# Optimization experiments

Hardware: AMD Instinct MI355X
Metric: run time of the kernel (lower is better)

## Reference

```python
import jax, jax.numpy as jnp
import numpy as np

DIM = 768
N_HEADS = 12
HEAD_DIM = DIM // N_HEADS
B, S = 2, 4096


def setup_inputs() -> dict:
    key = jax.random.key(0)
    k_x, k_wqkv, k_bqkv, k_wout, k_bout = jax.random.split(key, 5)
    scale_in = 1.0 / np.sqrt(DIM)
    return {
        "x": jax.random.normal(k_x, (B, S, DIM), dtype=jnp.float32),
        "Wqkv": jax.random.normal(k_wqkv, (DIM, 3 * DIM), dtype=jnp.float32) * scale_in,
        "bqkv": jax.random.normal(k_bqkv, (3 * DIM,), dtype=jnp.float32) * 0.02,
        "Wout": jax.random.normal(k_wout, (DIM, DIM), dtype=jnp.float32) * scale_in,
        "bout": jax.random.normal(k_bout, (DIM,), dtype=jnp.float32) * 0.02,
    }


def reference(x, Wqkv, bqkv, Wout, bout):
    b, s, d = x.shape
    qkv = (x @ Wqkv + bqkv).reshape(b, s, 3, N_HEADS, HEAD_DIM)
    qkv = jnp.transpose(qkv, (2, 0, 3, 1, 4))  # [3, B, H, S, hd]
    q, k, v = qkv[0], qkv[1], qkv[2]
    scale = HEAD_DIM ** -0.5
    attn = jnp.einsum('bhqd,bhkd->bhqk', q, k) * scale  # [B, H, S, S]
    causal_mask = jnp.triu(jnp.ones((s, s), dtype=bool), k=1)
    attn = jnp.where(causal_mask[None, None], -jnp.inf, attn)
    attn = jax.nn.softmax(attn, axis=-1)
    out = jnp.einsum('bhqk,bhkd->bhqd', attn, v)  # [B, H, S, hd]
    out = jnp.transpose(out, (0, 2, 1, 3)).reshape(b, s, d)
    return out @ Wout + bout
```

## Files before the change

### kernel.cpp

```cpp
#include <hip/hip_runtime.h>
#include <hip/hip_bf16.h>
#include <math.h>

#define DIM 768
#define NH 12
#define HD 64
#define BATCH 2
#define SEQ 4096
#define MTOT (BATCH * SEQ)

#define QSCALE 0.1803368801111244f

typedef unsigned short u16;
typedef __bf16 bf16x8 __attribute__((ext_vector_type(8)));
typedef float  f32x4  __attribute__((ext_vector_type(4)));
typedef float  f32x16 __attribute__((ext_vector_type(16)));
typedef unsigned short u16x4 __attribute__((ext_vector_type(4)));
typedef unsigned short u16x8 __attribute__((ext_vector_type(8)));
typedef unsigned u32x4 __attribute__((ext_vector_type(4)));

__device__ inline u16 f2bf(float f) {
    unsigned u = __builtin_bit_cast(unsigned, f);
    u += 0x7fffu + ((u >> 16) & 1u);
    return (u16)(u >> 16);
}

#if defined(__has_builtin) && __has_builtin(__builtin_amdgcn_cvt_pk_bf16_f32)
#define HAVE_PK_BF16 1
__device__ inline unsigned pk2bf(float a, float b) {
    auto v = __builtin_amdgcn_cvt_pk_bf16_f32(a, b);
    return __builtin_bit_cast(unsigned, v);
}
#else
#define HAVE_PK_BF16 0
__device__ inline unsigned pk2bf(float a, float b) {
    return (unsigned)f2bf(a) | ((unsigned)f2bf(b) << 16);
}
#endif

__device__ inline f32x4 mfma16(bf16x8 a, bf16x8 b, f32x4 c) {
    return __builtin_amdgcn_mfma_f32_16x16x32_bf16(a, b, c, 0, 0, 0);
}
__device__ inline f32x16 mfma32(bf16x8 a, bf16x8 b, f32x16 c) {
    return __builtin_amdgcn_mfma_f32_32x32x16_bf16(a, b, c, 0, 0, 0);
}

__device__ inline void gl2lds16(const u16* g, u16* l) {
    __builtin_amdgcn_global_load_lds(
        (const __attribute__((address_space(1))) void*)g,
        (__attribute__((address_space(3))) void*)l,
        16, 0, 0);
}

__global__ __launch_bounds__(256)
void cvt_bf16(const float* __restrict__ src, u16* __restrict__ dst, int n8)
{
    int i = blockIdx.x * 256 + threadIdx.x;
    if (i >= n8) return;
    float4 a = ((const float4*)src)[i * 2];
    float4 b = ((const float4*)src)[i * 2 + 1];
    u16x8 o;
    o[0] = f2bf(a.x); o[1] = f2bf(a.y); o[2] = f2bf(a.z); o[3] = f2bf(a.w);
    o[4] = f2bf(b.x); o[5] = f2bf(b.y); o[6] = f2bf(b.z); o[7] = f2bf(b.w);
    ((u16x8*)dst)[i] = o;
}

__global__ __launch_bounds__(256)
void transpose_to_bf16(const float* __restrict__ src, u16* __restrict__ dst,
                       int R, int C)
{
    __shared__ float tile[32][33];
    const int c0 = blockIdx.x * 32, r0 = blockIdx.y * 32;
    const int tx = threadIdx.x & 31, ty = threadIdx.x >> 5;
#pragma unroll
    for (int i = 0; i < 4; ++i) {
        int row = ty * 4 + i;
        tile[row][tx] = src[(size_t)(r0 + row) * C + c0 + tx];
    }
    __syncthreads();
#pragma unroll
    for (int i = 0; i < 4; ++i) {
        int crow = ty * 4 + i;
        dst[(size_t)(c0 + crow) * R + r0 + tx] = f2bf(tile[tx][crow]);
    }
}

__device__ inline void gemm_lds_mainloop(const u16* __restrict__ Ag,
                                         const u16* __restrict__ Bg,
                                         int m0, int n0, int w, int lane,
                                         u16 (*As)[64 * 64], u16 (*Bs)[64 * 64],
                                         f32x4 acc[4][4])
{
    const int quad = lane >> 4, lc = lane & 15;
    const int wm = (w & 1) * 64, wn = (w >> 1) * 64;
    const int drow = lane >> 3;
    const int dp   = lane & 7;

#pragma unroll
    for (int mi = 0; mi < 4; ++mi)
#pragma unroll
        for (int nj = 0; nj < 4; ++nj)
            acc[mi][nj] = f32x4{0.f, 0.f, 0.f, 0.f};

#pragma unroll
    for (int i = 0; i < 2; ++i) {
        const int r  = w * 16 + i * 8 + drow;
        const int g  = dp ^ (r & 7);
        const int tr = 2 * r + (g >> 2);
        const int kc = g & 3;
        gl2lds16(Ag + (size_t)(m0 + tr) * 768 + kc * 8, &As[0][(w * 16 + i * 8) * 64]);
        gl2lds16(Bg + (size_t)(n0 + tr) * 768 + kc * 8, &Bs[0][(w * 16 + i * 8) * 64]);
    }
    __syncthreads();

    for (int ks = 0; ks < 24; ++ks) {
        const int cur = ks & 1;

        if (ks < 23) {
            const int k0n = (ks + 1) * 32;
#pragma unroll
            for (int i = 0; i < 2; ++i) {
                const int r  = w * 16 + i * 8 + drow;
                const int g  = dp ^ (r & 7);
                const int tr = 2 * r + (g >> 2);
                const int kc = g & 3;
                gl2lds16(Ag + (size_t)(m0 + tr) * 768 + k0n + kc * 8,
                         &As[1 - cur][(w * 16 + i * 8) * 64]);
                gl2lds16(Bg + (size_t)(n0 + tr) * 768 + k0n + kc * 8,
                         &Bs[1 - cur][(w * 16 + i * 8) * 64]);
            }
        }

        bf16x8 af[4], bfr[4];
#pragma unroll
        for (int mi = 0; mi < 4; ++mi) {
            const int m = wm + mi * 16 + lc;
            const int r = m >> 1;
            const int p = (((m & 1) * 4 + quad)) ^ (r & 7);
            af[mi] = *(const bf16x8*)&As[cur][r * 64 + p * 8];
        }
#pragma unroll
        for (int nj = 0; nj < 4; ++nj) {
            const int n = wn + nj * 16 + lc;
            const int r = n >> 1;
            const int p = (((n & 1) * 4 + quad)) ^ (r & 7);
            bfr[nj] = *(const bf16x8*)&Bs[cur][r * 64 + p * 8];
        }

#pragma unroll
        for (int mi = 0; mi < 4; ++mi)
#pragma unroll
            for (int nj = 0; nj < 4; ++nj)
                acc[mi][nj] = mfma16(af[mi], bfr[nj], acc[mi][nj]);

        __syncthreads();
    }
}

__global__ __launch_bounds__(256)
void gemm_qkv_mfma(const u16* __restrict__ A, const u16* __restrict__ Bt,
                   const float* __restrict__ bias,
                   u16* __restrict__ Qb, u16* __restrict__ Kb, u16* __restrict__ Vt)
{
    __shared__ u16 As[2][64 * 64];
    __shared__ u16 Bs[2][64 * 64];
    const int m0 = blockIdx.x * 128;
    const int n0 = blockIdx.y * 128;
    const int t = threadIdx.x;
    const int w = t >> 6, lane = t & 63;
    const int quad = lane >> 4, lc = lane & 15;
    const int wm = (w & 1) * 64, wn = (w >> 1) * 64;

    f32x4 acc[4][4];
    gemm_lds_mainloop(A, Bt, m0, n0, w, lane, As, Bs, acc);

    const int b  = m0 >> 12;
    const int s0 = (m0 & 4095) + wm;
    const int nbase = n0 + wn;
    const int three = nbase / 768;
    const int rem   = nbase - three * 768;
    const int h     = rem >> 6;
    const int bh    = b * NH + h;

    if (three < 2) {
        u16* dst = (three == 0) ? Qb : Kb;
        const float qs = (three == 0) ? QSCALE : 1.0f;
#pragma unroll
        for (int nj = 0; nj < 4; ++nj) {
            const float bi = bias[nbase + nj * 16 + lc];
            const int d = nj * 16 + lc;
#pragma unroll
            for (int mi = 0; mi < 4; ++mi) {
                const int s = s0 + mi * 16 + quad * 4;
#pragma unroll
                for (int r = 0; r < 4; ++r)
                    dst[((size_t)bh * SEQ + s + r) * HD + d] = f2bf((acc[mi][nj][r] + bi) * qs);
            }
        }
    } else {
#pragma unroll
        for (int nj = 0; nj < 4; ++nj) {
            const float bi = bias[nbase + nj * 16 + lc];
            const int d = nj * 16 + lc;
            const size_t rowb = ((size_t)bh * HD + d) * SEQ;
#pragma unroll
            for (int mi = 0; mi < 4; ++mi) {
                const int s = s0 + mi * 16 + quad * 4;
                u16x4 wv;
#pragma unroll
                for (int r = 0; r < 4; ++r) wv[r] = f2bf(acc[mi][nj][r] + bi);
                *(u16x4*)&Vt[rowb + s] = wv;
            }
        }
    }
}

__global__ __launch_bounds__(256)
void gemm_out_mfma(const u16* __restrict__ A, const u16* __restrict__ Bt,
                   const float* __restrict__ bias, float* __restrict__ C)
{
    __shared__ u16 As[2][64 * 64];
    __shared__ u16 Bs[2][64 * 64];
    const int m0 = blockIdx.x * 128;
    const int n0 = blockIdx.y * 128;
    const int t = threadIdx.x;
    const int w = t >> 6, lane = t & 63;
    const int quad = lane >> 4, lc = lane & 15;
    const int wm = (w & 1) * 64, wn = (w >> 1) * 64;

    f32x4 acc[4][4];
    gemm_lds_mainloop(A, Bt, m0, n0, w, lane, As, Bs, acc);

#pragma unroll
    for (int nj = 0; nj < 4; ++nj) {
        const int col = n0 + wn + nj * 16 + lc;
        const float bi = bias[col];
#pragma unroll
        for (int mi = 0; mi < 4; ++mi) {
            const int row = m0 + wm + mi * 16 + quad * 4;
#pragma unroll
            for (int r = 0; r < 4; ++r)
                C[(size_t)(row + r) * 768 + col] = acc[mi][nj][r] + bi;
        }
    }
}

__global__ __launch_bounds__(256, 4)
void flash_attn(const u16* __restrict__ Qg, const u16* __restrict__ Kg,
                const u16* __restrict__ Vtg, u16* __restrict__ Og)
{
    const int bh   = blockIdx.x;
    const int qt   = 63 - (int)blockIdx.y;
    const int b    = bh / NH, h = bh % NH;
    const int t    = threadIdx.x;
    const int w    = t >> 6;
    const int wq   = w >> 1;
    const int wk   = w & 1;
    const int lane = t & 63;
    const int lc32 = lane & 31;
    const int hi   = lane >> 5;
    const int drow = lane >> 3;
    const int dp   = lane & 7;

    __shared__ u16 Ks[2][64 * 64];
    __shared__ u16 Vs[2][64 * 64];

    const u16* Qp = Qg  + (size_t)bh * SEQ * HD;
    const u16* Kp = Kg  + (size_t)bh * SEQ * HD;
    const u16* Vp = Vtg + (size_t)bh * HD * SEQ;
    float* Vscr = (float*)&Vs[0][0];
    float* Lx   = (float*)&Ks[0][0];

    const int qrow0 = qt * 64 + wq * 32;

    bf16x8 qa[4];
#pragma unroll
    for (int ds = 0; ds < 4; ++ds)
        qa[ds] = *(const bf16x8*)
            &Qp[(size_t)(qrow0 + lc32) * HD + ds * 16 + hi * 8];

    f32x16 o2[2];
    o2[0] = f32x16{};
    o2[1] = f32x16{};
    float l_r = 0.f;

#pragma unroll
    for (int i = 0; i < 2; ++i) {
        const int r0  = w * 16 + i * 8;
        const int row = r0 + drow;
        const int gc  = dp ^ (row & 7);
        gl2lds16(Kp + (size_t)row * HD + gc * 8, &Ks[0][r0 * 64]);
        gl2lds16(Vp + (size_t)row * SEQ + gc * 8, &Vs[0][r0 * 64]);
    }
    __syncthreads();

    for (int tk = 0; tk <= qt; ++tk) {
        const int kb  = tk * 64;
        const int cur = tk & 1;

        if (tk < qt) {
            const int kbn = kb + 64;
#pragma unroll
            for (int i = 0; i < 2; ++i) {
                const int r0  = w * 16 + i * 8;
                const int row = r0 + drow;
                const int gc  = dp ^ (row & 7);
                gl2lds16(Kp + (size_t)(kbn + row) * HD + gc * 8,
                         &Ks[1 - cur][r0 * 64]);
                gl2lds16(Vp + (size_t)row * SEQ + kbn + gc * 8,
                         &Vs[1 - cur][r0 * 64]);
            }
        }

        f32x16 sacc = {};
        {
            const int row = wk * 32 + lc32;
            const int sw  = row & 7;
            __builtin_amdgcn_s_setprio(1);
#pragma unroll
            for (int ds = 0; ds < 4; ++ds) {
                bf16x8 kf = *(const bf16x8*)
                    &Ks[cur][row * 64 + (((ds * 2 + hi) ^ sw) * 8)];
                sacc = mfma32(kf, qa[ds], sacc);
            }
            __builtin_amdgcn_s_setprio(0);
        }

        if (tk == qt) {
            const int q = qrow0 + lc32;
#pragma unroll
            for (int r = 0; r < 16; ++r) {
                const int key = kb + wk * 32 + (r & 3) + 8 * (r >> 2) + 4 * hi;
                if (key > q) sacc[r] = -1e30f;
            }
        }

        float pv[16];
#pragma unroll
        for (int r = 0; r < 16; ++r)
            pv[r] = __builtin_amdgcn_exp2f(sacc[r]);

        l_r += (((pv[0] + pv[1]) + (pv[2] + pv[3]))
              + ((pv[4] + pv[5]) + (pv[6] + pv[7])))
             + (((pv[8] + pv[9]) + (pv[10] + pv[11]))
              + ((pv[12] + pv[13]) + (pv[14] + pv[15])));

        bf16x8 pa[2];
#pragma unroll
        for (int s = 0; s < 2; ++s) {
            unsigned w0 = pk2bf(pv[8 * s + 0], pv[8 * s + 1]);
            unsigned w1 = pk2bf(pv[8 * s + 2], pv[8 * s + 3]);
            unsigned w2 = pk2bf(pv[8 * s + 4], pv[8 * s + 5]);
            unsigned w3 = pk2bf(pv[8 * s + 6], pv[8 * s + 7]);
            asm("v_permlane32_swap_b32 %0, %1" : "+v"(w0), "+v"(w2));
            asm("v_permlane32_swap_b32 %0, %1" : "+v"(w1), "+v"(w3));
            u32x4 tw;
            tw[0] = w0; tw[1] = w1; tw[2] = w2; tw[3] = w3;
            pa[s] = __builtin_bit_cast(bf16x8, tw);
        }

        __builtin_amdgcn_s_setprio(1);
#pragma unroll
        for (int dt = 0; dt < 2; ++dt) {
            const int row = dt * 32 + lc32;
            const int sw  = row & 7;
#pragma unroll
            for (int s = 0; s < 2; ++s) {
                bf16x8 vf = *(const bf16x8*)
                    &Vs[cur][row * 64 + (((wk * 4 + s * 2 + hi) ^ sw) * 8)];
                o2[dt] = mfma32(pa[s], vf, o2[dt]);
            }
        }
        __builtin_amdgcn_s_setprio(0);

        __syncthreads();
    }

    const float lt = l_r + __shfl_xor(l_r, 32);

    if (wk == 1) {
#pragma unroll
        for (int dt = 0; dt < 2; ++dt)
#pragma unroll
            for (int r = 0; r < 16; ++r) {
                const int ql = (r & 3) + 8 * (r >> 2) + 4 * hi;
                Vscr[wq * 2048 + ql * 64 + dt * 32 + lc32] = o2[dt][r];
            }
        if (lane < 32) Lx[wq * 32 + lc32] = lt;
    }
    __syncthreads();
    if (wk == 0) {
        const float linv_q = 1.0f / (lt + Lx[wq * 32 + lc32]);
#pragma unroll
        for (int r = 0; r < 16; ++r) {
            const int ql   = (r & 3) + 8 * (r >> 2) + 4 * hi;
            const float li = __shfl(linv_q, ql);
            const int q = qrow0 + ql;
            const size_t base = ((size_t)(b * SEQ + q)) * DIM + h * HD + lc32;
#pragma unroll
            for (int dt = 0; dt < 2; ++dt) {
                const float ov = o2[dt][r]
                    + Vscr[wq * 2048 + ql * 64 + dt * 32 + lc32];
                Og[base + dt * 32] = f2bf(ov * li);
            }
        }
    }
}

extern "C" void kernel_launch(void* const* d_in, const int* in_sizes, int n_in,
                              void* d_out, int out_size, void* d_ws, size_t ws_size,
                              hipStream_t stream)
{
    const float* x    = (const float*)d_in[0];
    const float* Wqkv = (const float*)d_in[1];
    const float* bqkv = (const float*)d_in[2];
    const float* Wout = (const float*)d_in[3];
    const float* bout = (const float*)d_in[4];
    float* out = (float*)d_out;

    const size_t NX  = (size_t)MTOT * DIM;
    const size_t NWQ = (size_t)DIM * 3 * DIM;
    const size_t NWO = (size_t)DIM * DIM;
    u16* p   = (u16*)d_ws;
    u16* Xb  = p;              p += NX;
    u16* Wqt = p;              p += NWQ;
    u16* Wot = p;              p += NWO;
    u16* Qb  = p;              p += NX;
    u16* Kb  = p;              p += NX;
    u16* Vt  = p;              p += NX;
    u16* Ao  = p;

    cvt_bf16<<<(int)(NX / 8 + 255) / 256, 256, 0, stream>>>(x, Xb, (int)(NX / 8));
    transpose_to_bf16<<<dim3(2304 / 32, 768 / 32), 256, 0, stream>>>(Wqkv, Wqt, 768, 2304);
    transpose_to_bf16<<<dim3(768 / 32, 768 / 32), 256, 0, stream>>>(Wout, Wot, 768, 768);

    gemm_qkv_mfma<<<dim3(MTOT / 128, 2304 / 128), 256, 0, stream>>>(Xb, Wqt, bqkv, Qb, Kb, Vt);
    flash_attn<<<dim3(24, 64), 256, 0, stream>>>(Qb, Kb, Vt, Ao);
    gemm_out_mfma<<<dim3(MTOT / 128, 768 / 128), 256, 0, stream>>>(Ao, Wot, bout, out);
}
```

Baseline: 239.6 us.

## Load K and V fragments directly from global memory, dropping LDS staging

```diff
diff --git a/kernel.cpp b/kernel.cpp
--- a/kernel.cpp
+++ b/kernel.cpp
@@ -259,19 +259,16 @@
     const int lane = t & 63;
     const int lc32 = lane & 31;
     const int hi   = lane >> 5;
-    const int drow = lane >> 3;
-    const int dp   = lane & 7;
-
-    __shared__ u16 Ks[2][64 * 64];
-    __shared__ u16 Vs[2][64 * 64];
+
+    __shared__ float Vscr[4096];
+    __shared__ float Lx[64];
 
     const u16* Qp = Qg  + (size_t)bh * SEQ * HD;
     const u16* Kp = Kg  + (size_t)bh * SEQ * HD;
     const u16* Vp = Vtg + (size_t)bh * HD * SEQ;
-    float* Vscr = (float*)&Vs[0][0];
-    float* Lx   = (float*)&Ks[0][0];
 
     const int qrow0 = qt * 64 + wq * 32;
+    const int krow  = wk * 32 + lc32;
 
     bf16x8 qa[4];
 #pragma unroll
@@ -284,43 +281,20 @@
     o2[1] = f32x16{};
     float l_r = 0.f;
 
-#pragma unroll
-    for (int i = 0; i < 2; ++i) {
-        const int r0  = w * 16 + i * 8;
-        const int row = r0 + drow;
-        const int gc  = dp ^ (row & 7);
-        gl2lds16(Kp + (size_t)row * HD + gc * 8, &Ks[0][r0 * 64]);
-        gl2lds16(Vp + (size_t)row * SEQ + gc * 8, &Vs[0][r0 * 64]);
-    }
-    __syncthreads();
+    const u16* Krow = Kp + (size_t)krow * HD;
+    const u16* V0   = Vp + (size_t)(lc32)      * SEQ + wk * 32 + hi * 8;
+    const u16* V1   = Vp + (size_t)(32 + lc32) * SEQ + wk * 32 + hi * 8;
 
     for (int tk = 0; tk <= qt; ++tk) {
-        const int kb  = tk * 64;
-        const int cur = tk & 1;
-
-        if (tk < qt) {
-            const int kbn = kb + 64;
-#pragma unroll
-            for (int i = 0; i < 2; ++i) {
-                const int r0  = w * 16 + i * 8;
-                const int row = r0 + drow;
-                const int gc  = dp ^ (row & 7);
-                gl2lds16(Kp + (size_t)(kbn + row) * HD + gc * 8,
-                         &Ks[1 - cur][r0 * 64]);
-                gl2lds16(Vp + (size_t)row * SEQ + kbn + gc * 8,
-                         &Vs[1 - cur][r0 * 64]);
-            }
-        }
+        const int kb = tk * 64;
 
         f32x16 sacc = {};
         {
-            const int row = wk * 32 + lc32;
-            const int sw  = row & 7;
+            const u16* kp = Krow + (size_t)kb * HD;
             __builtin_amdgcn_s_setprio(1);
 #pragma unroll
             for (int ds = 0; ds < 4; ++ds) {
-                bf16x8 kf = *(const bf16x8*)
-                    &Ks[cur][row * 64 + (((ds * 2 + hi) ^ sw) * 8)];
+                bf16x8 kf = *(const bf16x8*)&kp[ds * 16 + hi * 8];
                 sacc = mfma32(kf, qa[ds], sacc);
             }
             __builtin_amdgcn_s_setprio(0);
@@ -361,19 +335,13 @@
 
         __builtin_amdgcn_s_setprio(1);
 #pragma unroll
-        for (int dt = 0; dt < 2; ++dt) {
-            const int row = dt * 32 + lc32;
-            const int sw  = row & 7;
-#pragma unroll
-            for (int s = 0; s < 2; ++s) {
-                bf16x8 vf = *(const bf16x8*)
-                    &Vs[cur][row * 64 + (((wk * 4 + s * 2 + hi) ^ sw) * 8)];
-                o2[dt] = mfma32(pa[s], vf, o2[dt]);
-            }
+        for (int s = 0; s < 2; ++s) {
+            bf16x8 vf0 = *(const bf16x8*)&V0[kb + s * 16];
+            bf16x8 vf1 = *(const bf16x8*)&V1[kb + s * 16];
+            o2[0] = mfma32(pa[s], vf0, o2[0]);
+            o2[1] = mfma32(pa[s], vf1, o2[1]);
         }
         __builtin_amdgcn_s_setprio(0);
-
-        __syncthreads();
     }
 
     const float lt = l_r + __shfl_xor(l_r, 32);
```

Result: slower. 354.6 us (+48.0%).
